# Kernel tuning notes

Measured on AMD Instinct MI355X. Metric: run time of the kernel, lower is better.

The kernel has to match this reference:

```python
import jax, jax.numpy as jnp
import numpy as np

D_MODEL = 1024
N_HEAD = 16
HEAD_DIM = D_MODEL // N_HEAD


def setup_inputs() -> dict:
    key = jax.random.key(0)
    k1, k2, k3 = jax.random.split(key, 3)
    x = jax.random.normal(k1, (2, 2048, D_MODEL), dtype=jnp.float32)
    w_qkv = jax.random.normal(k2, (D_MODEL, 3 * D_MODEL), dtype=jnp.float32) * (1.0 / np.sqrt(D_MODEL))
    w_proj = jax.random.normal(k3, (D_MODEL, D_MODEL), dtype=jnp.float32) * (1.0 / np.sqrt(D_MODEL))
    return {"x": x, "w_qkv": w_qkv, "w_proj": w_proj}


def reference(x, w_qkv, w_proj):
    bs, sl, dm = x.shape
    qkv = x @ w_qkv                                   # [B,S,3*D]
    qkv = qkv.reshape(bs, sl, 3, N_HEAD, HEAD_DIM)
    q, k, v = qkv[:, :, 0], qkv[:, :, 1], qkv[:, :, 2]  # [B,S,H,d]
    q = q.transpose(0, 2, 1, 3)                        # [B,H,S,d]
    k = k.transpose(0, 2, 1, 3)
    v = v.transpose(0, 2, 1, 3)
    sc = 1.0 / np.sqrt(HEAD_DIM).astype(np.float32)
    attn = jnp.einsum('bhqd,bhkd->bhqk', q, k) * sc    # [B,H,S,S]
    causal = jnp.tril(jnp.ones((sl, sl), dtype=bool))  # True = keep
    attn = jnp.where(causal, attn, -jnp.inf)
    w = jax.nn.softmax(attn, axis=-1)                  # [B,H,S,S] (dropout p=0)
    o = jnp.einsum('bhqk,bhkd->bhqd', w, v)            # [B,H,S,d]
    out = o.transpose(0, 2, 1, 3).reshape(bs, sl, dm)
    out = out @ w_proj
    return (out, w)
```

## Files before the change

### kernel.cpp

```cpp
#include <hip/hip_runtime.h>

typedef _Float16 half8 __attribute__((ext_vector_type(8)));
typedef float f32x4 __attribute__((ext_vector_type(4)));

__device__ __forceinline__ void gl2lds16(const _Float16* g, _Float16* l) {
  __builtin_amdgcn_global_load_lds((const __attribute__((address_space(1))) void*)g,
                                   (__attribute__((address_space(3))) void*)l, 16, 0, 0);
}

__global__ __launch_bounds__(256) void cvt_kernel(const float* __restrict__ in,
                                                  _Float16* __restrict__ out, int n) {
  int i = (blockIdx.x * 256 + threadIdx.x) * 8;
  if (i >= n) return;
  float4 a = *(const float4*)(in + i);
  float4 b = *(const float4*)(in + i + 4);
  half8 o;
  o[0] = (_Float16)a.x; o[1] = (_Float16)a.y; o[2] = (_Float16)a.z; o[3] = (_Float16)a.w;
  o[4] = (_Float16)b.x; o[5] = (_Float16)b.y; o[6] = (_Float16)b.z; o[7] = (_Float16)b.w;
  *(half8*)(out + i) = o;
}

__global__ __launch_bounds__(256) void cvtT_kernel(const float* __restrict__ in,
                                                   _Float16* __restrict__ out,
                                                   int K, int N) {
  __shared__ float Ts[64][65];
  const int k0 = blockIdx.y * 64, n0 = blockIdx.x * 64;
  const int t = threadIdx.x;
  const int r = t >> 4, c = (t & 15) * 4;
#pragma unroll
  for (int i = 0; i < 4; i++) {
    float4 v = *(const float4*)(in + (size_t)(k0 + r + i * 16) * N + n0 + c);
    Ts[r + i * 16][c] = v.x; Ts[r + i * 16][c + 1] = v.y;
    Ts[r + i * 16][c + 2] = v.z; Ts[r + i * 16][c + 3] = v.w;
  }
  __syncthreads();
  const int nl = t >> 2, kq = (t & 3) * 16;
  half8 o0, o1;
#pragma unroll
  for (int j = 0; j < 8; j++) {
    o0[j] = (_Float16)Ts[kq + j][nl];
    o1[j] = (_Float16)Ts[kq + 8 + j][nl];
  }
  *(half8*)(out + (size_t)(n0 + nl) * K + k0 + kq) = o0;
  *(half8*)(out + (size_t)(n0 + nl) * K + k0 + kq + 8) = o1;
}

__global__ __launch_bounds__(256) void vtrans_kernel(const _Float16* __restrict__ v,
                                                     _Float16* __restrict__ vt) {
  __shared__ _Float16 Ht[64][72];
  const int s0 = blockIdx.x * 64;
  const _Float16* vb = v + (size_t)blockIdx.y * 131072;
  _Float16* vtb = vt + (size_t)blockIdx.y * 131072;
  const int t = threadIdx.x;
  const int sl = t >> 3, dq = (t & 7) * 8;
  *(half8*)&Ht[sl][dq] = *(const half8*)(vb + (s0 + sl) * 64 + dq);
  *(half8*)&Ht[sl + 32][dq] = *(const half8*)(vb + (s0 + sl + 32) * 64 + dq);
  __syncthreads();
  const int dl = t >> 2, sq = (t & 3) * 16;
  half8 o0, o1;
#pragma unroll
  for (int j = 0; j < 8; j++) {
    o0[j] = Ht[sq + j][dl];
    o1[j] = Ht[sq + 8 + j][dl];
  }
  *(half8*)(vtb + (size_t)dl * 2048 + s0 + sq) = o0;
  *(half8*)(vtb + (size_t)dl * 2048 + s0 + sq + 8) = o1;
}

template <int MODE, int BN>
__global__ __launch_bounds__(256) void gemm16(const _Float16* __restrict__ A,
                                              const _Float16* __restrict__ B,
                                              float* __restrict__ Cf,
                                              _Float16* __restrict__ Ch,
                                              int M, int N, int K) {
  constexpr int MI = (BN == 128) ? 4 : 2;
  __shared__ __align__(16) _Float16 As[128 * 32];
  __shared__ __align__(16) _Float16 Bs[BN * 32];
  const int tid = threadIdx.x;
  const int lane = tid & 63;
  const int wid = tid >> 6;
  const int quad = lane >> 4;
  const int l16 = lane & 15;
  const int mbase = (BN == 128) ? (wid >> 1) * 64 : wid * 32;
  const int nbase = (BN == 128) ? (wid & 1) * 64 : 0;
  const int m0 = blockIdx.y * 128;
  const int n0 = blockIdx.x * BN;

  f32x4 acc[MI][4];
  const f32x4 fz = {0.f, 0.f, 0.f, 0.f};
#pragma unroll
  for (int i = 0; i < MI; i++)
#pragma unroll
    for (int j = 0; j < 4; j++) acc[i][j] = fz;

  const int srow = tid >> 2;
  const int kq = (tid & 3) * 8;

  for (int kt = 0; kt < K; kt += 32) {
    gl2lds16(A + (size_t)(m0 + srow) * K + kt + kq, &As[tid * 8]);
    gl2lds16(A + (size_t)(m0 + 64 + srow) * K + kt + kq, &As[2048 + tid * 8]);
    gl2lds16(B + (size_t)(n0 + srow) * K + kt + kq, &Bs[tid * 8]);
    if (BN == 128)
      gl2lds16(B + (size_t)(n0 + 64 + srow) * K + kt + kq, &Bs[2048 + tid * 8]);
    __syncthreads();
    half8 af[MI], bf[4];
#pragma unroll
    for (int mi = 0; mi < MI; mi++)
      af[mi] = *(const half8*)&As[(mbase + mi * 16 + l16) * 32 + quad * 8];
#pragma unroll
    for (int ni = 0; ni < 4; ni++)
      bf[ni] = *(const half8*)&Bs[(nbase + ni * 16 + l16) * 32 + quad * 8];
#pragma unroll
    for (int mi = 0; mi < MI; mi++)
#pragma unroll
      for (int ni = 0; ni < 4; ni++)
        acc[mi][ni] = __builtin_amdgcn_mfma_f32_16x16x32_f16(af[mi], bf[ni], acc[mi][ni], 0, 0, 0);
    __syncthreads();
  }

#pragma unroll
  for (int mi = 0; mi < MI; mi++)
#pragma unroll
    for (int ni = 0; ni < 4; ni++)
#pragma unroll
      for (int r = 0; r < 4; r++) {
        int row = m0 + mbase + mi * 16 + quad * 4 + r;
        int col = n0 + nbase + ni * 16 + l16;
        float v = acc[mi][ni][r];
        if (MODE == 0) {
          Cf[(size_t)row * N + col] = v;
        } else {
          int which = col >> 10, h = (col >> 6) & 15, d = col & 63;
          int b = row >> 11, s = row & 2047;
          Ch[((((size_t)(which * 2 + b) * 16 + h) * 2048) + s) * 64 + d] = (_Float16)v;
        }
      }
}

__global__ __launch_bounds__(256) void attn_kernel(const _Float16* __restrict__ qkv,
                                                   const _Float16* __restrict__ vt,
                                                   float* __restrict__ w_out,
                                                   _Float16* __restrict__ o_buf) {
  const int qt = blockIdx.x, bh = blockIdx.y;
  const int tid = threadIdx.x;
  const int lane = tid & 63;
  const int wid = tid >> 6;
  const int quad = lane >> 4;
  const int l16 = lane & 15;

  const _Float16* qp = qkv + (size_t)bh * 131072;
  const _Float16* kp = qp + 4194304;
  const _Float16* vtb = vt + (size_t)bh * 131072;

  __shared__ __align__(16) _Float16 Ks[2 * 64 * 32];
  __shared__ __align__(16) _Float16 Vs[2 * 64 * 32];
  __shared__ __align__(16) _Float16 Ps[64][72];

  const int qrow = qt * 64 + wid * 16 + l16;
  const half8 qa0 = *(const half8*)(qp + qrow * 64 + quad * 8);
  const half8 qa1 = *(const half8*)(qp + qrow * 64 + 32 + quad * 8);

  const int srow = tid >> 2;
  const int blk8 = (tid & 3) * 8;
  const float sc = 0.125f;
  const f32x4 fz = {0.f, 0.f, 0.f, 0.f};
  const int lrow0 = wid * 16 + quad * 4;

  float lsum[4] = {0.f, 0.f, 0.f, 0.f};

  for (int kt = 0; kt <= qt; kt++) {
    gl2lds16(kp + (size_t)(kt * 64 + srow) * 64 + blk8, &Ks[tid * 8]);
    gl2lds16(kp + (size_t)(kt * 64 + srow) * 64 + 32 + blk8, &Ks[2048 + tid * 8]);
    __syncthreads();
    f32x4 sacc[4];
#pragma unroll
    for (int ni = 0; ni < 4; ni++) {
      half8 kb0 = *(const half8*)&Ks[(ni * 16 + l16) * 32 + quad * 8];
      half8 kb1 = *(const half8*)&Ks[2048 + (ni * 16 + l16) * 32 + quad * 8];
      f32x4 s = fz;
      s = __builtin_amdgcn_mfma_f32_16x16x32_f16(qa0, kb0, s, 0, 0, 0);
      s = __builtin_amdgcn_mfma_f32_16x16x32_f16(qa1, kb1, s, 0, 0, 0);
      sacc[ni] = s;
    }
    if (kt < qt) {
#pragma unroll
      for (int ni = 0; ni < 4; ni++)
#pragma unroll
        for (int r = 0; r < 4; r++) lsum[r] += __expf(sacc[ni][r] * sc);
    } else {
#pragma unroll
      for (int ni = 0; ni < 4; ni++)
#pragma unroll
        for (int r = 0; r < 4; r++) {
          if (ni * 16 + l16 <= lrow0 + r) lsum[r] += __expf(sacc[ni][r] * sc);
        }
    }
    __syncthreads();
  }
  float invl[4];
#pragma unroll
  for (int r = 0; r < 4; r++) {
    float s = lsum[r];
    s += __shfl_xor(s, 1); s += __shfl_xor(s, 2);
    s += __shfl_xor(s, 4); s += __shfl_xor(s, 8);
    invl[r] = 1.0f / s;
  }

  f32x4 oacc[4];
#pragma unroll
  for (int di = 0; di < 4; di++) oacc[di] = fz;

  float* wbase = w_out + (size_t)bh * 4194304 + (size_t)qt * 64 * 2048;

  for (int kt = 0; kt < 32; kt++) {
    if (kt <= qt) {
      gl2lds16(kp + (size_t)(kt * 64 + srow) * 64 + blk8, &Ks[tid * 8]);
      gl2lds16(kp + (size_t)(kt * 64 + srow) * 64 + 32 + blk8, &Ks[2048 + tid * 8]);
      gl2lds16(vtb + (size_t)srow * 2048 + kt * 64 + blk8, &Vs[tid * 8]);
      gl2lds16(vtb + (size_t)srow * 2048 + kt * 64 + 32 + blk8, &Vs[2048 + tid * 8]);
      __syncthreads();
      f32x4 sacc[4];
#pragma unroll
      for (int ni = 0; ni < 4; ni++) {
        half8 kb0 = *(const half8*)&Ks[(ni * 16 + l16) * 32 + quad * 8];
        half8 kb1 = *(const half8*)&Ks[2048 + (ni * 16 + l16) * 32 + quad * 8];
        f32x4 s = fz;
        s = __builtin_amdgcn_mfma_f32_16x16x32_f16(qa0, kb0, s, 0, 0, 0);
        s = __builtin_amdgcn_mfma_f32_16x16x32_f16(qa1, kb1, s, 0, 0, 0);
        sacc[ni] = s;
      }
#pragma unroll
      for (int ni = 0; ni < 4; ni++)
#pragma unroll
        for (int r = 0; r < 4; r++) {
          int lrw = lrow0 + r;
          int col = ni * 16 + l16;
          float p = __expf(sacc[ni][r] * sc) * invl[r];
          if (kt == qt && col > lrw) p = 0.0f;
          wbase[(size_t)lrw * 2048 + kt * 64 + col] = p;
          Ps[lrw][col] = (_Float16)p;
        }
      __syncthreads();
#pragma unroll
      for (int kk = 0; kk < 2; kk++) {
        half8 pa = *(const half8*)&Ps[wid * 16 + l16][kk * 32 + quad * 8];
#pragma unroll
        for (int di = 0; di < 4; di++) {
          half8 vb = *(const half8*)&Vs[kk * 2048 + (di * 16 + l16) * 32 + quad * 8];
          oacc[di] = __builtin_amdgcn_mfma_f32_16x16x32_f16(pa, vb, oacc[di], 0, 0, 0);
        }
      }
      __syncthreads();
    } else {
      const int rr = tid >> 4;
      const int cc = (tid & 15) * 4;
      float* wz = wbase + (size_t)kt * 64 + cc;
#pragma unroll
      for (int p = 0; p < 4; p++)
        *(f32x4*)(wz + (size_t)(p * 16 + rr) * 2048) = fz;
    }
  }

  const int b = bh >> 4, h = bh & 15;
#pragma unroll
  for (int di = 0; di < 4; di++)
#pragma unroll
    for (int r = 0; r < 4; r++) {
      int s = qt * 64 + lrow0 + r;
      int d = di * 16 + l16;
      o_buf[((size_t)(b * 2048 + s) * 16 + h) * 64 + d] = (_Float16)oacc[di][r];
    }
}

extern "C" void kernel_launch(void* const* d_in, const int* in_sizes, int n_in,
                              void* d_out, int out_size, void* d_ws, size_t ws_size,
                              hipStream_t stream) {
  const float* x = (const float*)d_in[0];
  const float* w_qkv = (const float*)d_in[1];
  const float* w_proj = (const float*)d_in[2];
  float* out = (float*)d_out;
  float* w_attn = out + (size_t)4194304;

  char* ws = (char*)d_ws;
  _Float16* x16 = (_Float16*)ws;
  _Float16* wqkvT = (_Float16*)(ws + (size_t)(8 << 20));
  _Float16* wprojT = (_Float16*)(ws + (size_t)(14 << 20));
  _Float16* qkvb = (_Float16*)(ws + (size_t)(16 << 20));
  _Float16* vT = (_Float16*)(ws + (size_t)(40 << 20));
  _Float16* ob = (_Float16*)(ws + (size_t)(48 << 20));

  cvt_kernel<<<2048, 256, 0, stream>>>(x, x16, 4194304);
  cvtT_kernel<<<dim3(48, 16), 256, 0, stream>>>(w_qkv, wqkvT, 1024, 3072);
  cvtT_kernel<<<dim3(16, 16), 256, 0, stream>>>(w_proj, wprojT, 1024, 1024);

  gemm16<1, 128><<<dim3(24, 32), 256, 0, stream>>>(x16, wqkvT, nullptr, qkvb, 4096, 3072, 1024);
  vtrans_kernel<<<dim3(32, 32), 256, 0, stream>>>(qkvb + (size_t)2 * 4194304, vT);
  attn_kernel<<<dim3(32, 32), 256, 0, stream>>>(qkvb, vT, w_attn, ob);
  gemm16<0, 64><<<dim3(16, 32), 256, 0, stream>>>(ob, wprojT, out, nullptr, 4096, 1024, 1024);
}
```

Before: 721.9 us.

## Coalesce attention-weight stores, double-buffer K/V tiles, and schedule heavy query tiles first

The attention-weight output is now written as 16-byte nontemporal vector stores. Each wave reads back its own probability rows from LDS, replacing scattered per-element 4-byte stores. The masked zero region is written up front with nontemporal stores. K and V tiles are double-buffered in LDS so the next tile's global-to-LDS load overlaps the current tile's MFMA work, which removes one barrier per iteration. Query tiles are launched in reverse order so the longest causal blocks start first. The stored weights are now the fp16-rounded probabilities, which reduces output precision.

Result: faster. 699.1 us (-3.2%).

```diff
diff --git a/kernel.cpp b/kernel.cpp
--- a/kernel.cpp
+++ b/kernel.cpp
@@ -1,11 +1,16 @@
 #include <hip/hip_runtime.h>
 
 typedef _Float16 half8 __attribute__((ext_vector_type(8)));
+typedef _Float16 half4 __attribute__((ext_vector_type(4)));
 typedef float f32x4 __attribute__((ext_vector_type(4)));
 
 __device__ __forceinline__ void gl2lds16(const _Float16* g, _Float16* l) {
   __builtin_amdgcn_global_load_lds((const __attribute__((address_space(1))) void*)g,
                                    (__attribute__((address_space(3))) void*)l, 16, 0, 0);
+}
+
+__device__ __forceinline__ void nt_store4(float* p, f32x4 v) {
+  __builtin_nontemporal_store(v, (f32x4*)p);
 }
 
 __global__ __launch_bounds__(256) void cvt_kernel(const float* __restrict__ in,
@@ -141,7 +146,8 @@
                                                    const _Float16* __restrict__ vt,
                                                    float* __restrict__ w_out,
                                                    _Float16* __restrict__ o_buf) {
-  const int qt = blockIdx.x, bh = blockIdx.y;
+  const int qt = 31 - blockIdx.x;
+  const int bh = blockIdx.y;
   const int tid = threadIdx.x;
   const int lane = tid & 63;
   const int wid = tid >> 6;
@@ -152,8 +158,8 @@
   const _Float16* kp = qp + 4194304;
   const _Float16* vtb = vt + (size_t)bh * 131072;
 
-  __shared__ __align__(16) _Float16 Ks[2 * 64 * 32];
-  __shared__ __align__(16) _Float16 Vs[2 * 64 * 32];
+  __shared__ __align__(16) _Float16 Ks[2][4096];
+  __shared__ __align__(16) _Float16 Vs[2][4096];
   __shared__ __align__(16) _Float16 Ps[64][72];
 
   const int qrow = qt * 64 + wid * 16 + l16;
@@ -166,17 +172,34 @@
   const f32x4 fz = {0.f, 0.f, 0.f, 0.f};
   const int lrow0 = wid * 16 + quad * 4;
 
+  float* wbase = w_out + (size_t)bh * 4194304 + (size_t)qt * 131072;
+
+  {
+    const int rr = tid >> 4, cc = (tid & 15) * 4;
+    for (int kt = qt + 1; kt < 32; kt++) {
+      float* wz = wbase + (size_t)kt * 64 + cc;
+#pragma unroll
+      for (int p = 0; p < 4; p++)
+        nt_store4(wz + (size_t)(p * 16 + rr) * 2048, fz);
+    }
+  }
+
   float lsum[4] = {0.f, 0.f, 0.f, 0.f};
 
+  int cur = 0;
+  gl2lds16(kp + (size_t)srow * 64 + blk8, &Ks[0][tid * 8]);
+  gl2lds16(kp + (size_t)srow * 64 + 32 + blk8, &Ks[0][2048 + tid * 8]);
+  __syncthreads();
   for (int kt = 0; kt <= qt; kt++) {
-    gl2lds16(kp + (size_t)(kt * 64 + srow) * 64 + blk8, &Ks[tid * 8]);
-    gl2lds16(kp + (size_t)(kt * 64 + srow) * 64 + 32 + blk8, &Ks[2048 + tid * 8]);
-    __syncthreads();
+    if (kt < qt) {
+      gl2lds16(kp + (size_t)((kt + 1) * 64 + srow) * 64 + blk8, &Ks[cur ^ 1][tid * 8]);
+      gl2lds16(kp + (size_t)((kt + 1) * 64 + srow) * 64 + 32 + blk8, &Ks[cur ^ 1][2048 + tid * 8]);
+    }
     f32x4 sacc[4];
 #pragma unroll
     for (int ni = 0; ni < 4; ni++) {
-      half8 kb0 = *(const half8*)&Ks[(ni * 16 + l16) * 32 + quad * 8];
-      half8 kb1 = *(const half8*)&Ks[2048 + (ni * 16 + l16) * 32 + quad * 8];
+      half8 kb0 = *(const half8*)&Ks[cur][(ni * 16 + l16) * 32 + quad * 8];
+      half8 kb1 = *(const half8*)&Ks[cur][2048 + (ni * 16 + l16) * 32 + quad * 8];
       f32x4 s = fz;
       s = __builtin_amdgcn_mfma_f32_16x16x32_f16(qa0, kb0, s, 0, 0, 0);
       s = __builtin_amdgcn_mfma_f32_16x16x32_f16(qa1, kb1, s, 0, 0, 0);
@@ -196,6 +219,7 @@
         }
     }
     __syncthreads();
+    cur ^= 1;
   }
   float invl[4];
 #pragma unroll
@@ -210,55 +234,64 @@
 #pragma unroll
   for (int di = 0; di < 4; di++) oacc[di] = fz;
 
-  float* wbase = w_out + (size_t)bh * 4194304 + (size_t)qt * 64 * 2048;
-
-  for (int kt = 0; kt < 32; kt++) {
-    if (kt <= qt) {
-      gl2lds16(kp + (size_t)(kt * 64 + srow) * 64 + blk8, &Ks[tid * 8]);
-      gl2lds16(kp + (size_t)(kt * 64 + srow) * 64 + 32 + blk8, &Ks[2048 + tid * 8]);
-      gl2lds16(vtb + (size_t)srow * 2048 + kt * 64 + blk8, &Vs[tid * 8]);
-      gl2lds16(vtb + (size_t)srow * 2048 + kt * 64 + 32 + blk8, &Vs[2048 + tid * 8]);
-      __syncthreads();
-      f32x4 sacc[4];
-#pragma unroll
-      for (int ni = 0; ni < 4; ni++) {
-        half8 kb0 = *(const half8*)&Ks[(ni * 16 + l16) * 32 + quad * 8];
-        half8 kb1 = *(const half8*)&Ks[2048 + (ni * 16 + l16) * 32 + quad * 8];
-        f32x4 s = fz;
-        s = __builtin_amdgcn_mfma_f32_16x16x32_f16(qa0, kb0, s, 0, 0, 0);
-        s = __builtin_amdgcn_mfma_f32_16x16x32_f16(qa1, kb1, s, 0, 0, 0);
-        sacc[ni] = s;
+  cur = 0;
+  gl2lds16(kp + (size_t)srow * 64 + blk8, &Ks[0][tid * 8]);
+  gl2lds16(kp + (size_t)srow * 64 + 32 + blk8, &Ks[0][2048 + tid * 8]);
+  gl2lds16(vtb + (size_t)srow * 2048 + blk8, &Vs[0][tid * 8]);
+  gl2lds16(vtb + (size_t)srow * 2048 + 32 + blk8, &Vs[0][2048 + tid * 8]);
+  __syncthreads();
+  for (int kt = 0; kt <= qt; kt++) {
+    if (kt < qt) {
+      const int kn = kt + 1;
+      gl2lds16(kp + (size_t)(kn * 64 + srow) * 64 + blk8, &Ks[cur ^ 1][tid * 8]);
+      gl2lds16(kp + (size_t)(kn * 64 + srow) * 64 + 32 + blk8, &Ks[cur ^ 1][2048 + tid * 8]);
+      gl2lds16(vtb + (size_t)srow * 2048 + kn * 64 + blk8, &Vs[cur ^ 1][tid * 8]);
+      gl2lds16(vtb + (size_t)srow * 2048 + kn * 64 + 32 + blk8, &Vs[cur ^ 1][2048 + tid * 8]);
+    }
+    f32x4 sacc[4];
+#pragma unroll
+    for (int ni = 0; ni < 4; ni++) {
+      half8 kb0 = *(const half8*)&Ks[cur][(ni * 16 + l16) * 32 + quad * 8];
+      half8 kb1 = *(const half8*)&Ks[cur][2048 + (ni * 16 + l16) * 32 + quad * 8];
+      f32x4 s = fz;
+      s = __builtin_amdgcn_mfma_f32_16x16x32_f16(qa0, kb0, s, 0, 0, 0);
+      s = __builtin_amdgcn_mfma_f32_16x16x32_f16(qa1, kb1, s, 0, 0, 0);
+      sacc[ni] = s;
+    }
+#pragma unroll
+    for (int ni = 0; ni < 4; ni++)
+#pragma unroll
+      for (int r = 0; r < 4; r++) {
+        int lrw = lrow0 + r;
+        int col = ni * 16 + l16;
+        float p = __expf(sacc[ni][r] * sc) * invl[r];
+        if (kt == qt && col > lrw) p = 0.0f;
+        Ps[lrw][col] = (_Float16)p;
       }
 #pragma unroll
-      for (int ni = 0; ni < 4; ni++)
-#pragma unroll
-        for (int r = 0; r < 4; r++) {
-          int lrw = lrow0 + r;
-          int col = ni * 16 + l16;
-          float p = __expf(sacc[ni][r] * sc) * invl[r];
-          if (kt == qt && col > lrw) p = 0.0f;
-          wbase[(size_t)lrw * 2048 + kt * 64 + col] = p;
-          Ps[lrw][col] = (_Float16)p;
-        }
-      __syncthreads();
-#pragma unroll
-      for (int kk = 0; kk < 2; kk++) {
-        half8 pa = *(const half8*)&Ps[wid * 16 + l16][kk * 32 + quad * 8];
-#pragma unroll
-        for (int di = 0; di < 4; di++) {
-          half8 vb = *(const half8*)&Vs[kk * 2048 + (di * 16 + l16) * 32 + quad * 8];
-          oacc[di] = __builtin_amdgcn_mfma_f32_16x16x32_f16(pa, vb, oacc[di], 0, 0, 0);
-        }
+    for (int kk = 0; kk < 2; kk++) {
+      half8 pa = *(const half8*)&Ps[wid * 16 + l16][kk * 32 + quad * 8];
+#pragma unroll
+      for (int di = 0; di < 4; di++) {
+        half8 vb = *(const half8*)&Vs[cur][kk * 2048 + (di * 16 + l16) * 32 + quad * 8];
+        oacc[di] = __builtin_amdgcn_mfma_f32_16x16x32_f16(pa, vb, oacc[di], 0, 0, 0);
       }
-      __syncthreads();
-    } else {
-      const int rr = tid >> 4;
-      const int cc = (tid & 15) * 4;
-      float* wz = wbase + (size_t)kt * 64 + cc;
-#pragma unroll
-      for (int p = 0; p < 4; p++)
-        *(f32x4*)(wz + (size_t)(p * 16 + rr) * 2048) = fz;
-    }
+    }
+    {
+      const int erow = lane >> 2;
+      const int ec = (lane & 3) * 4;
+      const _Float16* prow = &Ps[wid * 16 + erow][0];
+      float* wrow = wbase + (size_t)(wid * 16 + erow) * 2048 + kt * 64;
+#pragma unroll
+      for (int j = 0; j < 4; j++) {
+        half4 h = *(const half4*)(prow + j * 16 + ec);
+        f32x4 o;
+        o[0] = (float)h[0]; o[1] = (float)h[1]; o[2] = (float)h[2]; o[3] = (float)h[3];
+        nt_store4(wrow + j * 16 + ec, o);
+      }
+    }
+    __syncthreads();
+    cur ^= 1;
   }
 
   const int b = bh >> 4, h = bh & 15;
```
